# Kernel tuning notes

Measured on AMD Instinct MI355X. Metric: run time of the kernel, lower is better.

## Reference

```python
import jax, jax.numpy as jnp
import numpy as np

DIM = 512
NUM_HEADS = 8


def setup_inputs() -> dict:
    key = jax.random.key(0)
    ks = jax.random.split(key, 10)
    B, N, C = 2, 4096, DIM
    s = 0.02
    return {
        "x": jax.random.normal(ks[0], (B, N, C), dtype=jnp.float32),
        "Wq": jax.random.normal(ks[1], (C, C), dtype=jnp.float32) * s,
        "Wk": jax.random.normal(ks[2], (C, C), dtype=jnp.float32) * s,
        "Wv": jax.random.normal(ks[3], (C, C), dtype=jnp.float32) * s,
        "Wattn": jax.random.normal(ks[4], (C, C), dtype=jnp.float32) * s,
        "Wconv": jax.random.normal(ks[5], (C, C), dtype=jnp.float32) * s,
        "dw_kernel": jax.random.normal(ks[6], (C, 1, 3), dtype=jnp.float32) * s,  # depthwise (O, I/groups, K)
        "dw_bias": jax.random.normal(ks[7], (C,), dtype=jnp.float32) * s,
        "Wcout": jax.random.normal(ks[8], (C, C), dtype=jnp.float32) * s,
        "H": 8,
        "W": 512,
    }


def reference(x, Wq, Wk, Wv, Wattn, Wconv, dw_kernel, dw_bias, Wcout, H, W):
    B, N, C = x.shape
    nh = NUM_HEADS
    hd = C // nh
    scale = hd ** (-0.5)

    # QKV projections (torch Linear: x @ W.T), split heads -> [B, nh, N, hd]
    q = (x @ Wq.T).reshape(B, N, nh, hd).transpose(0, 2, 1, 3)
    k = (x @ Wk.T).reshape(B, N, nh, hd).transpose(0, 2, 1, 3)
    v = (x @ Wv.T).reshape(B, N, nh, hd).transpose(0, 2, 1, 3)

    # Materialized N x N attention (faithful to source)
    scores = jnp.einsum("bhqd,bhkd->bhqk", q, k) * scale
    weights = jax.nn.softmax(scores, axis=-1)
    attn = jnp.einsum("bhqk,bhkd->bhqd", weights, v)
    attn = attn.transpose(0, 2, 1, 3).reshape(B, N, C)
    attn_out = attn @ Wattn.T

    # Parallel depthwise-conv branch
    ci = (x @ Wconv.T).transpose(0, 2, 1)  # [B, C, N]
    co = jax.lax.conv_general_dilated(
        ci, dw_kernel,
        window_strides=(1,), padding=((1, 1),),
        feature_group_count=C,
        dimension_numbers=("NCH", "OIH", "NCH"),
    ) + dw_bias[None, :, None]
    conv_out = co.transpose(0, 2, 1) @ Wcout.T  # [B, N, C]

    out = attn_out + conv_out
    # NOTE: source shadows arg H with num_heads before the view
    return out.reshape(B, nh, W, C)
```

## Files before the change

### kernel.cpp

```cpp
#include <hip/hip_runtime.h>

typedef __attribute__((ext_vector_type(8))) short bf16x8;
typedef __attribute__((ext_vector_type(4))) short bf16x4;
typedef __attribute__((ext_vector_type(4))) float f32x4;

constexpr int kB = 2, kN = 4096, kC = 512, kNH = 8, kHD = 64;
constexpr int kBN = kB * kN;
constexpr int kWElems = 262144;
constexpr int kWAll = 6 * kWElems;
constexpr int kWExtra = 3584;
constexpr float kQScale = 0.1803368801f;

__device__ __forceinline__ short f2bf(float f) {
  union { float f; unsigned u; } v; v.f = f;
  unsigned r = v.u + 0x7fffu + ((v.u >> 16) & 1u);
  return (short)(r >> 16);
}
__device__ __forceinline__ float bf2f(short s) {
  union { unsigned u; float f; } v; v.u = ((unsigned)(unsigned short)s) << 16;
  return v.f;
}
__device__ __forceinline__ float exp2_(float x) {
#if __has_builtin(__builtin_amdgcn_exp2f)
  return __builtin_amdgcn_exp2f(x);
#else
  return exp2f(x);
#endif
}

__device__ __forceinline__ bf16x8 ld8(const short* p) { return *(const bf16x8*)p; }
__device__ __forceinline__ bf16x8 ld8(const float* p) {
  float4 a = *(const float4*)p;
  float4 b = *(const float4*)(p + 4);
  bf16x8 r;
  r[0] = f2bf(a.x); r[1] = f2bf(a.y); r[2] = f2bf(a.z); r[3] = f2bf(a.w);
  r[4] = f2bf(b.x); r[5] = f2bf(b.y); r[6] = f2bf(b.z); r[7] = f2bf(b.w);
  return r;
}
__device__ __forceinline__ void stf(short* p, float v) { *p = f2bf(v); }
__device__ __forceinline__ void stf(float* p, float v) { *p = v; }

__device__ __forceinline__ void gload_lds16(const void* g, void* l) {
  __builtin_amdgcn_global_load_lds(
      (const __attribute__((address_space(1))) void*)g,
      (__attribute__((address_space(3))) void*)l, 16, 0, 0);
}

__global__ void detect_dtype(const unsigned* __restrict__ x, int* __restrict__ flag) {
  const int lane = threadIdx.x & 63;
  unsigned w = x[lane];
  int e = (int)((w >> 7) & 0xffu);
  bool bf = (e >= 100 && e <= 140);
  unsigned long long m = __ballot(bf);
  if (lane == 0) *flag = (__popcll(m) >= 32) ? 1 : 0;
}

__global__ __launch_bounds__(256) void convert_weights(
    const void* Wq, const void* Wk, const void* Wv, const void* Wc,
    const void* Wa, const void* Wco, const void* dwk, const void* dwb,
    const int* __restrict__ flag, short* __restrict__ dst) {
  const int gtid = blockIdx.x * 256 + threadIdx.x;
  const bool bf = (*flag != 0);
  if (gtid < kWAll / 8) {
    const int e = gtid * 8;
    const int t = e >> 18, off = e & (kWElems - 1);
    const void* src = (t == 0) ? Wq : (t == 1) ? Wk : (t == 2) ? Wv
                    : (t == 3) ? Wc : (t == 4) ? Wa : Wco;
    bf16x8 v = bf ? ld8((const short*)src + off) : ld8((const float*)src + off);
    *(bf16x8*)(dst + e) = v;
  } else {
    const int eoff = gtid - kWAll / 8;
    if (eoff < 1536) {
      dst[kWAll + eoff] = bf ? ((const short*)dwk)[eoff]
                             : f2bf(((const float*)dwk)[eoff]);
    } else if (eoff < 2048) {
      const int i = eoff - 1536;
      dst[kWAll + 1536 + i] = bf ? ((const short*)dwb)[i]
                                 : f2bf(((const float*)dwb)[i]);
    } else if (eoff < 2048 + 1536) {
      const int t2 = eoff - 2048;
      const int tap = t2 >> 9, c = t2 & 511;
      dst[kWAll + 2048 + t2] = bf ? ((const short*)dwk)[c * 3 + tap]
                                  : f2bf(((const float*)dwk)[c * 3 + tap]);
    }
  }
}

__global__ __launch_bounds__(256) void convert_x(
    const void* x, const int* __restrict__ flag, short* __restrict__ xb) {
  const int i = (blockIdx.x * 256 + threadIdx.x) * 8;
  bf16x8 v = (*flag) ? ld8((const short*)x + i) : ld8((const float*)x + i);
  *(bf16x8*)(xb + i) = v;
}

__global__ __launch_bounds__(256, 3) void proj_gemm(
    const short* __restrict__ xb, const short* __restrict__ wb,
    short* __restrict__ q, short* __restrict__ k, short* __restrict__ vT,
    short* __restrict__ ci) {
  __shared__ __align__(16) short As[128 * 32];
  __shared__ __align__(16) short Bs[128 * 32];
  const int t = threadIdx.x;
  const int wave = t >> 6, lane = t & 63;
  const int row = lane & 15, quad = lane >> 4;
  const int bn = blockIdx.x & 15;
  const int bm = blockIdx.x >> 4;
  const int m0 = bm * 128, n0 = bn * 128;
  const int wm = wave & 1, wn = wave >> 1;
  const int srow = lane >> 2, schunk = lane & 3;

  f32x4 acc[4][4];
#pragma unroll
  for (int mi = 0; mi < 4; ++mi)
#pragma unroll
    for (int ni = 0; ni < 4; ++ni)
#pragma unroll
      for (int r = 0; r < 4; ++r) acc[mi][ni][r] = 0.0f;

  for (int k0 = 0; k0 < kC; k0 += 32) {
    const short* ga = xb + (size_t)(m0 + wave * 32 + srow) * kC + k0 + schunk * 8;
    const short* gb = wb + (size_t)(n0 + wave * 32 + srow) * kC + k0 + schunk * 8;
    gload_lds16(ga,            &As[(wave * 32) * 32]);
    gload_lds16(ga + 16 * kC,  &As[(wave * 32 + 16) * 32]);
    gload_lds16(gb,            &Bs[(wave * 32) * 32]);
    gload_lds16(gb + 16 * kC,  &Bs[(wave * 32 + 16) * 32]);
    __syncthreads();

    bf16x8 af[4], bfr[4];
#pragma unroll
    for (int mi = 0; mi < 4; ++mi)
      af[mi] = *(const bf16x8*)(&As[(wm * 64 + mi * 16 + row) * 32 + quad * 8]);
#pragma unroll
    for (int ni = 0; ni < 4; ++ni)
      bfr[ni] = *(const bf16x8*)(&Bs[(wn * 64 + ni * 16 + row) * 32 + quad * 8]);
#pragma unroll
    for (int mi = 0; mi < 4; ++mi)
#pragma unroll
      for (int ni = 0; ni < 4; ++ni)
        acc[mi][ni] = __builtin_amdgcn_mfma_f32_16x16x32_bf16(
            af[mi], bfr[ni], acc[mi][ni], 0, 0, 0);
    __syncthreads();
  }

  const int gc0 = n0 + wn * 64;
  const int mat = gc0 >> 9;
  const float scale = (mat == 0) ? kQScale : 1.0f;
#pragma unroll
  for (int mi = 0; mi < 4; ++mi) {
#pragma unroll
    for (int ni = 0; ni < 4; ++ni) {
#pragma unroll
      for (int r = 0; r < 4; ++r) {
        const int gm = m0 + wm * 64 + mi * 16 + quad * 4 + r;
        const int c_ = ((gc0 + ni * 16) & 511) + row;
        const int b_ = gm >> 12;
        const int n_ = gm & (kN - 1);
        const short bv = f2bf(acc[mi][ni][r] * scale);
        if (mat == 3) {
          ci[(b_ * kN + n_) * kC + c_] = bv;
        } else {
          const int h = c_ >> 6, d = c_ & 63;
          const int bh = b_ * kNH + h;
          if (mat == 0)      q[(bh * kN + n_) * kHD + d] = bv;
          else if (mat == 1) k[(bh * kN + n_) * kHD + d] = bv;
          else               vT[(bh * kHD + d) * kN + n_] = bv;
        }
      }
    }
  }
}

__global__ __launch_bounds__(256) void dwconv(
    const short* __restrict__ ci, const short* __restrict__ wb,
    short* __restrict__ cb) {
  const int e0 = (blockIdx.x * 256 + threadIdx.x) * 8;
  const int c0 = e0 & (kC - 1);
  const int bn = e0 >> 9;
  const int n_ = bn & (kN - 1);
  bf16x8 xc = ld8(ci + e0);
  bf16x8 xm, xp;
  if (n_ > 0) xm = ld8(ci + e0 - kC);
  else
#pragma unroll
    for (int i = 0; i < 8; ++i) xm[i] = 0;
  if (n_ < kN - 1) xp = ld8(ci + e0 + kC);
  else
#pragma unroll
    for (int i = 0; i < 8; ++i) xp[i] = 0;
  bf16x8 w0 = ld8(wb + kWAll + 2048 + c0);
  bf16x8 w1 = ld8(wb + kWAll + 2048 + 512 + c0);
  bf16x8 w2 = ld8(wb + kWAll + 2048 + 1024 + c0);
  bf16x8 bi = ld8(wb + kWAll + 1536 + c0);
  bf16x8 o;
#pragma unroll
  for (int i = 0; i < 8; ++i) {
    float a = bf2f(bi[i]) + bf2f(xm[i]) * bf2f(w0[i]) +
              bf2f(xc[i]) * bf2f(w1[i]) + bf2f(xp[i]) * bf2f(w2[i]);
    o[i] = f2bf(a);
  }
  *(bf16x8*)(cb + e0) = o;
}

__global__ __launch_bounds__(256, 3) void attn_flash(
    const short* __restrict__ q, const short* __restrict__ k,
    const short* __restrict__ vT, short* __restrict__ attn) {
  __shared__ __align__(16) short Kb[2][64 * 72];
  __shared__ __align__(16) short Vb[64 * 72];
  const int t = threadIdx.x;
  const int wave = t >> 6;
  const int lane = t & 63;
  const int row = lane & 15;
  const int quad = lane >> 4;

  const int slot = blockIdx.x & 7;
  const int inner = blockIdx.x >> 3;
  const int bh = slot * 2 + (inner & 1);
  const int q0 = (inner >> 1) * 128 + wave * 32;

  const short* qbase = q + (bh * kN + q0) * kHD;
  const short* kbase = k + bh * kN * kHD;
  const short* vbase = vT + bh * kHD * kN;

  bf16x8 qb[2][2];
#pragma unroll
  for (int g = 0; g < 2; ++g) {
    qb[g][0] = *(const bf16x8*)(qbase + (g * 16 + row) * kHD + quad * 8);
    qb[g][1] = *(const bf16x8*)(qbase + (g * 16 + row) * kHD + 32 + quad * 8);
  }

  f32x4 o[2][4];
#pragma unroll
  for (int g = 0; g < 2; ++g)
#pragma unroll
    for (int j = 0; j < 4; ++j)
#pragma unroll
      for (int r = 0; r < 4; ++r) o[g][j][r] = 0.0f;
  float l_[2] = {0.0f, 0.0f};

  const int i0 = t, i1 = t + 256;
  const int sr0 = i0 >> 3, sc0 = i0 & 7;
  const int sr1 = i1 >> 3, sc1 = i1 & 7;

  {
    bf16x8 ka = *(const bf16x8*)(kbase + i0 * 8);
    bf16x8 kb2 = *(const bf16x8*)(kbase + i1 * 8);
    *(bf16x8*)(&Kb[0][sr0 * 72 + sc0 * 8]) = ka;
    *(bf16x8*)(&Kb[0][sr1 * 72 + sc1 * 8]) = kb2;
  }
  __syncthreads();

  for (int kt = 0; kt < kN / 64; ++kt) {
    const int cur = kt & 1;
    bf16x8 v0 = *(const bf16x8*)(vbase + sr0 * kN + kt * 64 + sc0 * 8);
    bf16x8 v1 = *(const bf16x8*)(vbase + sr1 * kN + kt * 64 + sc1 * 8);
    bf16x8 kn0, kn1;
    if (kt < kN / 64 - 1) {
      kn0 = *(const bf16x8*)(kbase + (kt + 1) * 4096 + i0 * 8);
      kn1 = *(const bf16x8*)(kbase + (kt + 1) * 4096 + i1 * 8);
    }

    f32x4 s[2][4];
#pragma unroll
    for (int g = 0; g < 2; ++g)
#pragma unroll
      for (int jk = 0; jk < 4; ++jk)
#pragma unroll
        for (int r = 0; r < 4; ++r) s[g][jk][r] = 0.0f;
#pragma unroll
    for (int jk = 0; jk < 4; ++jk) {
      const short* kr = &Kb[cur][(jk * 16 + row) * 72 + quad * 8];
      bf16x8 a0 = *(const bf16x8*)kr;
      bf16x8 a1 = *(const bf16x8*)(kr + 32);
#pragma unroll
      for (int g = 0; g < 2; ++g) {
        s[g][jk] = __builtin_amdgcn_mfma_f32_16x16x32_bf16(a0, qb[g][0], s[g][jk], 0, 0, 0);
        s[g][jk] = __builtin_amdgcn_mfma_f32_16x16x32_bf16(a1, qb[g][1], s[g][jk], 0, 0, 0);
      }
    }

    bf16x8 pb[2][2];
#pragma unroll
    for (int g = 0; g < 2; ++g) {
      float rs = 0.0f;
#pragma unroll
      for (int jk = 0; jk < 4; ++jk)
#pragma unroll
        for (int r = 0; r < 4; ++r) {
          float p = exp2_(s[g][jk][r]);
          s[g][jk][r] = p;
          rs += p;
        }
      l_[g] += rs;
#pragma unroll
      for (int c = 0; c < 2; ++c)
#pragma unroll
        for (int j = 0; j < 4; ++j) {
          pb[g][c][j]     = f2bf(s[g][2 * c][j]);
          pb[g][c][j + 4] = f2bf(s[g][2 * c + 1][j]);
        }
    }

    *(bf16x8*)(&Vb[sr0 * 72 + sc0 * 8]) = v0;
    *(bf16x8*)(&Vb[sr1 * 72 + sc1 * 8]) = v1;
    __syncthreads();

#pragma unroll
    for (int jd = 0; jd < 4; ++jd) {
      const short* vb = &Vb[(jd * 16 + row) * 72 + quad * 4];
#pragma unroll
      for (int c = 0; c < 2; ++c) {
        bf16x4 lo = *(const bf16x4*)(vb + c * 32);
        bf16x4 hi = *(const bf16x4*)(vb + c * 32 + 16);
        bf16x8 av = __builtin_shufflevector(lo, hi, 0, 1, 2, 3, 4, 5, 6, 7);
#pragma unroll
        for (int g = 0; g < 2; ++g)
          o[g][jd] = __builtin_amdgcn_mfma_f32_16x16x32_bf16(
              av, pb[g][c], o[g][jd], 0, 0, 0);
      }
    }

    if (kt < kN / 64 - 1) {
      *(bf16x8*)(&Kb[1 - cur][sr0 * 72 + sc0 * 8]) = kn0;
      *(bf16x8*)(&Kb[1 - cur][sr1 * 72 + sc1 * 8]) = kn1;
    }
    __syncthreads();
  }

  const int b_ = bh >> 3, h = bh & 7;
#pragma unroll
  for (int g = 0; g < 2; ++g) {
    float lt = l_[g];
    lt += __shfl_xor(lt, 16);
    lt += __shfl_xor(lt, 32);
    const float linv = 1.0f / lt;
    const int n_ = q0 + g * 16 + row;
    short* ob = attn + (b_ * kN + n_) * kC + h * kHD + quad * 4;
#pragma unroll
    for (int jd = 0; jd < 4; ++jd) {
      short4 st = make_short4(f2bf(o[g][jd][0] * linv), f2bf(o[g][jd][1] * linv),
                              f2bf(o[g][jd][2] * linv), f2bf(o[g][jd][3] * linv));
      *(short4*)(ob + jd * 16) = st;
    }
  }
}

template <typename TO>
__device__ __forceinline__ void out_body(
    const short* __restrict__ attn, const short* __restrict__ cb,
    const short* __restrict__ wb, TO* __restrict__ out) {
  __shared__ __align__(16) short As[128 * 32];
  __shared__ __align__(16) short Bs[64 * 32];
  const int t = threadIdx.x;
  const int wave = t >> 6, lane = t & 63;
  const int row = lane & 15, quad = lane >> 4;
  const int bn = blockIdx.x & 7;
  const int bm = blockIdx.x >> 3;
  const int m0 = bm * 128, n0 = bn * 64;
  const int wm = wave & 1, wn = wave >> 1;
  const int srow = lane >> 2, schunk = lane & 3;

  f32x4 acc[4][2];
#pragma unroll
  for (int mi = 0; mi < 4; ++mi)
#pragma unroll
    for (int ni = 0; ni < 2; ++ni)
#pragma unroll
      for (int r = 0; r < 4; ++r) acc[mi][ni][r] = 0.0f;

  const short* Wa = wb + 4 * kWElems;
  const short* Wo = wb + 5 * kWElems;

  for (int k0 = 0; k0 < 1024; k0 += 32) {
    const short* Asrc = (k0 < 512) ? attn : cb;
    const short* Bsrc = (k0 < 512) ? Wa : Wo;
    const int ka = k0 & 511;
    const short* ga = Asrc + (size_t)(m0 + wave * 32 + srow) * kC + ka + schunk * 8;
    gload_lds16(ga,            &As[(wave * 32) * 32]);
    gload_lds16(ga + 16 * kC,  &As[(wave * 32 + 16) * 32]);
    const short* gb = Bsrc + (size_t)(n0 + wave * 16 + srow) * kC + ka + schunk * 8;
    gload_lds16(gb, &Bs[(wave * 16) * 32]);
    __syncthreads();

    bf16x8 af[4], bfr[2];
#pragma unroll
    for (int mi = 0; mi < 4; ++mi)
      af[mi] = *(const bf16x8*)(&As[(wm * 64 + mi * 16 + row) * 32 + quad * 8]);
#pragma unroll
    for (int ni = 0; ni < 2; ++ni)
      bfr[ni] = *(const bf16x8*)(&Bs[(wn * 32 + ni * 16 + row) * 32 + quad * 8]);
#pragma unroll
    for (int mi = 0; mi < 4; ++mi)
#pragma unroll
      for (int ni = 0; ni < 2; ++ni)
        acc[mi][ni] = __builtin_amdgcn_mfma_f32_16x16x32_bf16(
            af[mi], bfr[ni], acc[mi][ni], 0, 0, 0);
    __syncthreads();
  }

#pragma unroll
  for (int mi = 0; mi < 4; ++mi)
#pragma unroll
    for (int ni = 0; ni < 2; ++ni)
#pragma unroll
      for (int r = 0; r < 4; ++r) {
        const int gm = m0 + wm * 64 + mi * 16 + quad * 4 + r;
        const int gc = n0 + wn * 32 + ni * 16 + row;
        stf(out + (size_t)gm * kC + gc, acc[mi][ni][r]);
      }
}

__global__ __launch_bounds__(256, 4) void out_gemm(
    const short* __restrict__ attn, const short* __restrict__ cb,
    const short* __restrict__ wb, const int* __restrict__ flag, void* out) {
  if (*flag)
    out_body<short>(attn, cb, wb, (short*)out);
  else
    out_body<float>(attn, cb, wb, (float*)out);
}

extern "C" void kernel_launch(void* const* d_in, const int* in_sizes, int n_in,
                              void* d_out, int out_size, void* d_ws, size_t ws_size,
                              hipStream_t stream) {
  const void* x   = d_in[0];
  const void* Wq  = d_in[1];
  const void* Wk  = d_in[2];
  const void* Wv  = d_in[3];
  const void* Wa  = d_in[4];
  const void* Wc  = d_in[5];
  const void* dwk = d_in[6];
  const void* dwb = d_in[7];
  const void* Wco = d_in[8];

  short* ws = (short*)d_ws;
  const size_t E = (size_t)kBN * kC;
  int*   flag = (int*)ws;
  short* wb   = ws + 256;
  short* q    = wb + kWAll + kWExtra;
  short* k    = q + E;
  short* vT   = k + E;
  short* ci   = vT + E;
  short* cb   = ci + E;
  short* attn = ci;
  short* xb   = cb;

  detect_dtype<<<1, 64, 0, stream>>>((const unsigned*)x, flag);
  convert_weights<<<(kWAll / 8 + kWExtra + 255) / 256, 256, 0, stream>>>(
      Wq, Wk, Wv, Wc, Wa, Wco, dwk, dwb, flag, wb);
  convert_x<<<kBN * kC / (256 * 8), 256, 0, stream>>>(x, flag, xb);
  proj_gemm<<<1024, 256, 0, stream>>>(xb, wb, q, k, vT, ci);
  dwconv<<<(kBN * kC) / (256 * 8), 256, 0, stream>>>(ci, wb, cb);
  attn_flash<<<512, 256, 0, stream>>>(q, k, vT, attn);
  out_gemm<<<512, 256, 0, stream>>>(attn, cb, wb, flag, d_out);
}
```

Baseline: 267.1 us.

## Fuse conversion kernels, swizzle K=64 GEMM tiles, double-buffer V in attention

Merges the weight and x conversion kernels into a single launch. Both GEMMs now stage a K depth of 64 per iteration into XOR-swizzled LDS tiles, halving barrier count and avoiding bank conflicts. The flash attention kernel prefetches V one tile ahead into a double buffer with a pre-permuted layout, which removes a mid-loop barrier and allows single 16-byte LDS reads. P is packed to bf16 with a perm-based round-half-up conversion. The cost is more LDS per block, which may reduce occupancy.

```diff
diff --git a/kernel.cpp b/kernel.cpp
--- a/kernel.cpp
+++ b/kernel.cpp
@@ -1,7 +1,6 @@
 #include <hip/hip_runtime.h>
 
 typedef __attribute__((ext_vector_type(8))) short bf16x8;
-typedef __attribute__((ext_vector_type(4))) short bf16x4;
 typedef __attribute__((ext_vector_type(4))) float f32x4;
 
 constexpr int kB = 2, kN = 4096, kC = 512, kNH = 8, kHD = 64;
@@ -25,6 +24,14 @@
   return __builtin_amdgcn_exp2f(x);
 #else
   return exp2f(x);
+#endif
+}
+__device__ __forceinline__ unsigned pk2bf(float a, float b) {
+  union { float f; unsigned u; } ua, ub; ua.f = a; ub.f = b;
+#if __has_builtin(__builtin_amdgcn_perm)
+  return __builtin_amdgcn_perm(ub.u + 0x8000u, ua.u + 0x8000u, 0x07060302u);
+#else
+  return ((ua.u + 0x8000u) >> 16) | (((ub.u + 0x8000u) >> 16) << 16);
 #endif
 }
 
@@ -55,21 +62,24 @@
   if (lane == 0) *flag = (__popcll(m) >= 32) ? 1 : 0;
 }
 
-__global__ __launch_bounds__(256) void convert_weights(
+constexpr int kW8 = kWAll / 8;
+constexpr int kX8 = kBN * kC / 8;
+__global__ __launch_bounds__(256) void convert_all(
     const void* Wq, const void* Wk, const void* Wv, const void* Wc,
     const void* Wa, const void* Wco, const void* dwk, const void* dwb,
-    const int* __restrict__ flag, short* __restrict__ dst) {
+    const void* x, const int* __restrict__ flag, short* __restrict__ dst,
+    short* __restrict__ xb) {
   const int gtid = blockIdx.x * 256 + threadIdx.x;
   const bool bf = (*flag != 0);
-  if (gtid < kWAll / 8) {
+  if (gtid < kW8) {
     const int e = gtid * 8;
     const int t = e >> 18, off = e & (kWElems - 1);
     const void* src = (t == 0) ? Wq : (t == 1) ? Wk : (t == 2) ? Wv
                     : (t == 3) ? Wc : (t == 4) ? Wa : Wco;
     bf16x8 v = bf ? ld8((const short*)src + off) : ld8((const float*)src + off);
     *(bf16x8*)(dst + e) = v;
-  } else {
-    const int eoff = gtid - kWAll / 8;
+  } else if (gtid < kW8 + kWExtra) {
+    const int eoff = gtid - kW8;
     if (eoff < 1536) {
       dst[kWAll + eoff] = bf ? ((const short*)dwk)[eoff]
                              : f2bf(((const float*)dwk)[eoff]);
@@ -77,28 +87,25 @@
       const int i = eoff - 1536;
       dst[kWAll + 1536 + i] = bf ? ((const short*)dwb)[i]
                                  : f2bf(((const float*)dwb)[i]);
-    } else if (eoff < 2048 + 1536) {
+    } else {
       const int t2 = eoff - 2048;
       const int tap = t2 >> 9, c = t2 & 511;
       dst[kWAll + 2048 + t2] = bf ? ((const short*)dwk)[c * 3 + tap]
                                   : f2bf(((const float*)dwk)[c * 3 + tap]);
     }
-  }
-}
-
-__global__ __launch_bounds__(256) void convert_x(
-    const void* x, const int* __restrict__ flag, short* __restrict__ xb) {
-  const int i = (blockIdx.x * 256 + threadIdx.x) * 8;
-  bf16x8 v = (*flag) ? ld8((const short*)x + i) : ld8((const float*)x + i);
-  *(bf16x8*)(xb + i) = v;
+  } else if (gtid < kW8 + kWExtra + kX8) {
+    const int e = (gtid - kW8 - kWExtra) * 8;
+    bf16x8 v = bf ? ld8((const short*)x + e) : ld8((const float*)x + e);
+    *(bf16x8*)(xb + e) = v;
+  }
 }
 
 __global__ __launch_bounds__(256, 3) void proj_gemm(
     const short* __restrict__ xb, const short* __restrict__ wb,
     short* __restrict__ q, short* __restrict__ k, short* __restrict__ vT,
     short* __restrict__ ci) {
-  __shared__ __align__(16) short As[128 * 32];
-  __shared__ __align__(16) short Bs[128 * 32];
+  __shared__ __align__(16) short As[128 * 64];
+  __shared__ __align__(16) short Bs[128 * 64];
   const int t = threadIdx.x;
   const int wave = t >> 6, lane = t & 63;
   const int row = lane & 15, quad = lane >> 4;
@@ -106,7 +113,7 @@
   const int bm = blockIdx.x >> 4;
   const int m0 = bm * 128, n0 = bn * 128;
   const int wm = wave & 1, wn = wave >> 1;
-  const int srow = lane >> 2, schunk = lane & 3;
+  const int lrow = lane >> 3, lch = lane & 7;
 
   f32x4 acc[4][4];
 #pragma unroll
@@ -116,28 +123,40 @@
 #pragma unroll
       for (int r = 0; r < 4; ++r) acc[mi][ni][r] = 0.0f;
 
-  for (int k0 = 0; k0 < kC; k0 += 32) {
-    const short* ga = xb + (size_t)(m0 + wave * 32 + srow) * kC + k0 + schunk * 8;
-    const short* gb = wb + (size_t)(n0 + wave * 32 + srow) * kC + k0 + schunk * 8;
-    gload_lds16(ga,            &As[(wave * 32) * 32]);
-    gload_lds16(ga + 16 * kC,  &As[(wave * 32 + 16) * 32]);
-    gload_lds16(gb,            &Bs[(wave * 32) * 32]);
-    gload_lds16(gb + 16 * kC,  &Bs[(wave * 32 + 16) * 32]);
+  for (int k0 = 0; k0 < kC; k0 += 64) {
+#pragma unroll
+    for (int p = 0; p < 4; ++p) {
+      const int m = wave * 32 + p * 8 + lrow;
+      const int kch = lch ^ (m & 7);
+      gload_lds16(xb + (size_t)(m0 + m) * kC + k0 + kch * 8,
+                  &As[(wave * 32 + p * 8) * 64]);
+      gload_lds16(wb + (size_t)(n0 + m) * kC + k0 + kch * 8,
+                  &Bs[(wave * 32 + p * 8) * 64]);
+    }
     __syncthreads();
 
-    bf16x8 af[4], bfr[4];
-#pragma unroll
-    for (int mi = 0; mi < 4; ++mi)
-      af[mi] = *(const bf16x8*)(&As[(wm * 64 + mi * 16 + row) * 32 + quad * 8]);
-#pragma unroll
-    for (int ni = 0; ni < 4; ++ni)
-      bfr[ni] = *(const bf16x8*)(&Bs[(wn * 64 + ni * 16 + row) * 32 + quad * 8]);
-#pragma unroll
-    for (int mi = 0; mi < 4; ++mi)
-#pragma unroll
-      for (int ni = 0; ni < 4; ++ni)
-        acc[mi][ni] = __builtin_amdgcn_mfma_f32_16x16x32_bf16(
-            af[mi], bfr[ni], acc[mi][ni], 0, 0, 0);
+#pragma unroll
+    for (int kk2 = 0; kk2 < 2; ++kk2) {
+      bf16x8 af[4], bfr[4];
+#pragma unroll
+      for (int mi = 0; mi < 4; ++mi) {
+        const int m = wm * 64 + mi * 16 + row;
+        const int ch = (kk2 * 4 + quad) ^ (m & 7);
+        af[mi] = *(const bf16x8*)(&As[m * 64 + ch * 8]);
+      }
+#pragma unroll
+      for (int ni = 0; ni < 4; ++ni) {
+        const int n = wn * 64 + ni * 16 + row;
+        const int ch = (kk2 * 4 + quad) ^ (n & 7);
+        bfr[ni] = *(const bf16x8*)(&Bs[n * 64 + ch * 8]);
+      }
+#pragma unroll
+      for (int mi = 0; mi < 4; ++mi)
+#pragma unroll
+        for (int ni = 0; ni < 4; ++ni)
+          acc[mi][ni] = __builtin_amdgcn_mfma_f32_16x16x32_bf16(
+              af[mi], bfr[ni], acc[mi][ni], 0, 0, 0);
+    }
     __syncthreads();
   }
 
@@ -204,7 +223,7 @@
     const short* __restrict__ q, const short* __restrict__ k,
     const short* __restrict__ vT, short* __restrict__ attn) {
   __shared__ __align__(16) short Kb[2][64 * 72];
-  __shared__ __align__(16) short Vb[64 * 72];
+  __shared__ __align__(16) short VbS[2][64 * 72];
   const int t = threadIdx.x;
   const int wave = t >> 6;
   const int lane = t & 63;
@@ -239,23 +258,40 @@
   const int i0 = t, i1 = t + 256;
   const int sr0 = i0 >> 3, sc0 = i0 & 7;
   const int sr1 = i1 >> 3, sc1 = i1 & 7;
+  const int vb0 = (sc0 >> 2) * 32 + (sc0 & 1) * 16 + (sc0 & 2) * 2;
+  const int vb1 = (sc1 >> 2) * 32 + (sc1 & 1) * 16 + (sc1 & 2) * 2;
+
+  auto stage_v = [&](int buf, bf16x8 v0, bf16x8 v1) {
+    *(short4*)(&VbS[buf][sr0 * 72 + vb0]) =
+        make_short4(v0[0], v0[1], v0[2], v0[3]);
+    *(short4*)(&VbS[buf][sr0 * 72 + vb0 + 8]) =
+        make_short4(v0[4], v0[5], v0[6], v0[7]);
+    *(short4*)(&VbS[buf][sr1 * 72 + vb1]) =
+        make_short4(v1[0], v1[1], v1[2], v1[3]);
+    *(short4*)(&VbS[buf][sr1 * 72 + vb1 + 8]) =
+        make_short4(v1[4], v1[5], v1[6], v1[7]);
+  };
 
   {
     bf16x8 ka = *(const bf16x8*)(kbase + i0 * 8);
     bf16x8 kb2 = *(const bf16x8*)(kbase + i1 * 8);
     *(bf16x8*)(&Kb[0][sr0 * 72 + sc0 * 8]) = ka;
     *(bf16x8*)(&Kb[0][sr1 * 72 + sc1 * 8]) = kb2;
+    bf16x8 v0 = *(const bf16x8*)(vbase + sr0 * kN + sc0 * 8);
+    bf16x8 v1 = *(const bf16x8*)(vbase + sr1 * kN + sc1 * 8);
+    stage_v(0, v0, v1);
   }
   __syncthreads();
 
   for (int kt = 0; kt < kN / 64; ++kt) {
     const int cur = kt & 1;
-    bf16x8 v0 = *(const bf16x8*)(vbase + sr0 * kN + kt * 64 + sc0 * 8);
-    bf16x8 v1 = *(const bf16x8*)(vbase + sr1 * kN + kt * 64 + sc1 * 8);
-    bf16x8 kn0, kn1;
-    if (kt < kN / 64 - 1) {
+    const bool more = (kt < kN / 64 - 1);
+    bf16x8 kn0, kn1, vn0, vn1;
+    if (more) {
       kn0 = *(const bf16x8*)(kbase + (kt + 1) * 4096 + i0 * 8);
       kn1 = *(const bf16x8*)(kbase + (kt + 1) * 4096 + i1 * 8);
+      vn0 = *(const bf16x8*)(vbase + sr0 * kN + (kt + 1) * 64 + sc0 * 8);
+      vn1 = *(const bf16x8*)(vbase + sr1 * kN + (kt + 1) * 64 + sc1 * 8);
     }
 
     f32x4 s[2][4];
@@ -291,26 +327,22 @@
         }
       l_[g] += rs;
 #pragma unroll
-      for (int c = 0; c < 2; ++c)
-#pragma unroll
-        for (int j = 0; j < 4; ++j) {
-          pb[g][c][j]     = f2bf(s[g][2 * c][j]);
-          pb[g][c][j + 4] = f2bf(s[g][2 * c + 1][j]);
-        }
-    }
-
-    *(bf16x8*)(&Vb[sr0 * 72 + sc0 * 8]) = v0;
-    *(bf16x8*)(&Vb[sr1 * 72 + sc1 * 8]) = v1;
-    __syncthreads();
+      for (int c = 0; c < 2; ++c) {
+        union { unsigned u[4]; bf16x8 v; } pu;
+        pu.u[0] = pk2bf(s[g][2 * c][0], s[g][2 * c][1]);
+        pu.u[1] = pk2bf(s[g][2 * c][2], s[g][2 * c][3]);
+        pu.u[2] = pk2bf(s[g][2 * c + 1][0], s[g][2 * c + 1][1]);
+        pu.u[3] = pk2bf(s[g][2 * c + 1][2], s[g][2 * c + 1][3]);
+        pb[g][c] = pu.v;
+      }
+    }
 
 #pragma unroll
     for (int jd = 0; jd < 4; ++jd) {
-      const short* vb = &Vb[(jd * 16 + row) * 72 + quad * 4];
+      const short* vb = &VbS[cur][(jd * 16 + row) * 72 + quad * 8];
 #pragma unroll
       for (int c = 0; c < 2; ++c) {
-        bf16x4 lo = *(const bf16x4*)(vb + c * 32);
-        bf16x4 hi = *(const bf16x4*)(vb + c * 32 + 16);
-        bf16x8 av = __builtin_shufflevector(lo, hi, 0, 1, 2, 3, 4, 5, 6, 7);
+        bf16x8 av = *(const bf16x8*)(vb + c * 32);
 #pragma unroll
         for (int g = 0; g < 2; ++g)
           o[g][jd] = __builtin_amdgcn_mfma_f32_16x16x32_bf16(
@@ -318,9 +350,10 @@
       }
     }
 
-    if (kt < kN / 64 - 1) {
+    if (more) {
       *(bf16x8*)(&Kb[1 - cur][sr0 * 72 + sc0 * 8]) = kn0;
       *(bf16x8*)(&Kb[1 - cur][sr1 * 72 + sc1 * 8]) = kn1;
+      stage_v(1 - cur, vn0, vn1);
     }
     __syncthreads();
   }
@@ -347,8 +380,8 @@
 __device__ __forceinline__ void out_body(
     const short* __restrict__ attn, const short* __restrict__ cb,
     const short* __restrict__ wb, TO* __restrict__ out) {
-  __shared__ __align__(16) short As[128 * 32];
-  __shared__ __align__(16) short Bs[64 * 32];
+  __shared__ __align__(16) short As[128 * 64];
+  __shared__ __align__(16) short Bs[64 * 64];
   const int t = threadIdx.x;
   const int wave = t >> 6, lane = t & 63;
   const int row = lane & 15, quad = lane >> 4;
@@ -356,7 +389,7 @@
   const int bm = blockIdx.x >> 3;
   const int m0 = bm * 128, n0 = bn * 64;
   const int wm = wave & 1, wn = wave >> 1;
-  const int srow = lane >> 2, schunk = lane & 3;
+  const int lrow = lane >> 3, lch = lane & 7;
 
   f32x4 acc[4][2];
 #pragma unroll
@@ -369,30 +402,48 @@
   const short* Wa = wb + 4 * kWElems;
   const short* Wo = wb + 5 * kWElems;
 
-  for (int k0 = 0; k0 < 1024; k0 += 32) {
+  for (int k0 = 0; k0 < 1024; k0 += 64) {
     const short* Asrc = (k0 < 512) ? attn : cb;
     const short* Bsrc = (k0 < 512) ? Wa : Wo;
     const int ka = k0 & 511;
-    const short* ga = Asrc + (size_t)(m0 + wave * 32 + srow) * kC + ka + schunk * 8;
-    gload_lds16(ga,            &As[(wave * 32) * 32]);
-    gload_lds16(ga + 16 * kC,  &As[(wave * 32 + 16) * 32]);
-    const short* gb = Bsrc + (size_t)(n0 + wave * 16 + srow) * kC + ka + schunk * 8;
-    gload_lds16(gb, &Bs[(wave * 16) * 32]);
+#pragma unroll
+    for (int p = 0; p < 4; ++p) {
+      const int m = wave * 32 + p * 8 + lrow;
+      const int kch = lch ^ (m & 7);
+      gload_lds16(Asrc + (size_t)(m0 + m) * kC + ka + kch * 8,
+                  &As[(wave * 32 + p * 8) * 64]);
+    }
+#pragma unroll
+    for (int p = 0; p < 2; ++p) {
+      const int n = wave * 16 + p * 8 + lrow;
+      const int kch = lch ^ (n & 7);
+      gload_lds16(Bsrc + (size_t)(n0 + n) * kC + ka + kch * 8,
+                  &Bs[(wave * 16 + p * 8) * 64]);
+    }
     __syncthreads();
 
-    bf16x8 af[4], bfr[2];
-#pragma unroll
-    for (int mi = 0; mi < 4; ++mi)
-      af[mi] = *(const bf16x8*)(&As[(wm * 64 + mi * 16 + row) * 32 + quad * 8]);
-#pragma unroll
-    for (int ni = 0; ni < 2; ++ni)
-      bfr[ni] = *(const bf16x8*)(&Bs[(wn * 32 + ni * 16 + row) * 32 + quad * 8]);
-#pragma unroll
-    for (int mi = 0; mi < 4; ++mi)
-#pragma unroll
-      for (int ni = 0; ni < 2; ++ni)
-        acc[mi][ni] = __builtin_amdgcn_mfma_f32_16x16x32_bf16(
-            af[mi], bfr[ni], acc[mi][ni], 0, 0, 0);
+#pragma unroll
+    for (int kk2 = 0; kk2 < 2; ++kk2) {
+      bf16x8 af[4], bfr[2];
+#pragma unroll
+      for (int mi = 0; mi < 4; ++mi) {
+        const int m = wm * 64 + mi * 16 + row;
+        const int ch = (kk2 * 4 + quad) ^ (m & 7);
+        af[mi] = *(const bf16x8*)(&As[m * 64 + ch * 8]);
+      }
+#pragma unroll
+      for (int ni = 0; ni < 2; ++ni) {
+        const int n = wn * 32 + ni * 16 + row;
+        const int ch = (kk2 * 4 + quad) ^ (n & 7);
+        bfr[ni] = *(const bf16x8*)(&Bs[n * 64 + ch * 8]);
+      }
+#pragma unroll
+      for (int mi = 0; mi < 4; ++mi)
+#pragma unroll
+        for (int ni = 0; ni < 2; ++ni)
+          acc[mi][ni] = __builtin_amdgcn_mfma_f32_16x16x32_bf16(
+              af[mi], bfr[ni], acc[mi][ni], 0, 0, 0);
+    }
     __syncthreads();
   }
 
@@ -443,9 +494,9 @@
   short* xb   = cb;
 
   detect_dtype<<<1, 64, 0, stream>>>((const unsigned*)x, flag);
-  convert_weights<<<(kWAll / 8 + kWExtra + 255) / 256, 256, 0, stream>>>(
-      Wq, Wk, Wv, Wc, Wa, Wco, dwk, dwb, flag, wb);
-  convert_x<<<kBN * kC / (256 * 8), 256, 0, stream>>>(x, flag, xb);
+  const int cvt_threads = kW8 + kWExtra + kX8;
+  convert_all<<<(cvt_threads + 255) / 256, 256, 0, stream>>>(
+      Wq, Wk, Wv, Wc, Wa, Wco, dwk, dwb, x, flag, wb, xb);
   proj_gemm<<<1024, 256, 0, stream>>>(xb, wb, q, k, vT, ci);
   dwconv<<<(kBN * kC) / (256 * 8), 256, 0, stream>>>(ci, wb, cb);
   attn_flash<<<512, 256, 0, stream>>>(q, k, vT, attn);
```

New measurement: 245.9 us. 1.09x faster.
